# Kernel optimization log

Measured on AMD Instinct MI355X. Metric: run time of the kernel, lower is better.

Reference implementation:

```python
import jax, jax.numpy as jnp
import numpy as np

SMOOTHING = 0.9  # NEURON_CONFIG['signal_smoothing']
NUM_SOURCE = 16384
NUM_TARGET = 16384
NUM_BRANCHES = 64
BATCH = 32


def setup_inputs() -> dict:
    key = jax.random.key(0)
    k1, k2, k3, k4 = jax.random.split(key, 4)
    spikes = jax.random.normal(k1, (BATCH, NUM_SOURCE), dtype=jnp.float32)
    attenuation = jax.random.uniform(k2, (NUM_SOURCE, NUM_BRANCHES), dtype=jnp.float32)
    target_indices = jax.random.randint(k3, (NUM_SOURCE, NUM_BRANCHES), 0, NUM_TARGET)
    delays = jax.random.randint(k4, (NUM_SOURCE, NUM_BRANCHES), 0, 6)
    return {"spikes": spikes, "attenuation": attenuation,
            "target_indices": target_indices, "delays": delays}


def reference(spikes, attenuation, target_indices, delays):
    # spikes: [B, S]; attenuation/delays/target_indices: [S, Br]
    B = spikes.shape[0]
    num_target = NUM_TARGET
    att = jnp.clip(attenuation, 0.0, 1.0)
    decay = SMOOTHING ** delays.astype(spikes.dtype)          # [S, Br]
    # fused elementwise: signal per (batch, source, branch)
    signals = spikes[:, :, None] * (att * decay)[None, :, :]   # [B, S, Br]
    flat_t = target_indices.reshape(-1)                        # [S*Br]
    flat_s = signals.reshape(B, -1)                            # [B, S*Br]
    out = jnp.zeros((B, num_target), dtype=spikes.dtype)
    out = out.at[jnp.arange(B)[:, None], flat_t[None, :]].add(flat_s)
    return out
```

## Files before the change

### kernel.cpp

```cpp
#include <hip/hip_runtime.h>

#define S_  16384
#define T_  16384
#define B_  32
#define NEDGES (S_ * 64)
#define G_    256
#define NBKT  256
#define TPB   64
#define CAP_CELL  64
#define CAP_SPILL 64
#define CAP_BKT   6144

__device__ __forceinline__ float edge_weight(float a, int d) {
  float w = fminf(fmaxf(a, 0.0f), 1.0f);
  float r = (d & 1) ? 0.9f : 1.0f;
  r = (d & 2) ? r * 0.81f   : r;
  r = (d & 4) ? r * 0.6561f : r;
  return w * r;
}

__global__ __launch_bounds__(1024) void produce(
    const float* __restrict__ spikes,
    const float* __restrict__ att,
    const int*   __restrict__ tgt,
    const int*   __restrict__ del,
    float* __restrict__ spikesT,
    int2*  __restrict__ rec,
    int*   __restrict__ cntT,
    int*   __restrict__ spillCnt,
    int2*  __restrict__ spill) {
  __shared__ float tile[64][33];
  __shared__ int   cur[NBKT];
  __shared__ int   scur;
  const int g   = blockIdx.x;
  const int tid = threadIdx.x;

  if (tid < NBKT) cur[tid] = 0;
  if (tid == 0)   scur = 0;

  {
    const int x  = tid & 63;
    const int y  = tid >> 6;
    const int s0 = g * 64;
    tile[x][y]      = spikes[(size_t)y        * S_ + s0 + x];
    tile[x][y + 16] = spikes[(size_t)(y + 16) * S_ + s0 + x];
    __syncthreads();
    const int j = tid >> 5;
    const int b = tid & 31;
    spikesT[(size_t)(s0 + j)      * 32 + b] = tile[j][b];
    spikesT[(size_t)(s0 + j + 32) * 32 + b] = tile[j + 32][b];
  }

  const int e4  = g * 1024 + tid;
  int4   t = reinterpret_cast<const int4*>(tgt)[e4];
  float4 a = reinterpret_cast<const float4*>(att)[e4];
  int4   d = reinterpret_cast<const int4*>(del)[e4];
  const int src = (e4 * 4) >> 6;

#define EMIT(TV, AV, DV)                                                      \
  {                                                                           \
    const int bkt = (TV) >> 6;                                                \
    const int tl  = (TV) & 63;                                                \
    const int wb  = __float_as_int(edge_weight((AV), (DV)));                  \
    int slot = __hip_atomic_fetch_add(&cur[bkt], 1, __ATOMIC_RELAXED,         \
                                      __HIP_MEMORY_SCOPE_WORKGROUP);          \
    if (slot < CAP_CELL) {                                                    \
      rec[(((size_t)((bkt << 8) | g)) << 6) + slot] =                         \
          make_int2((tl << 14) | src, wb);                                    \
    } else {                                                                  \
      int sp = __hip_atomic_fetch_add(&scur, 1, __ATOMIC_RELAXED,             \
                                      __HIP_MEMORY_SCOPE_WORKGROUP);          \
      if (sp < CAP_SPILL)                                                     \
        spill[g * CAP_SPILL + sp] =                                           \
            make_int2((bkt << 20) | (tl << 14) | src, wb);                    \
    }                                                                         \
  }
  EMIT(t.x, a.x, d.x)
  EMIT(t.y, a.y, d.y)
  EMIT(t.z, a.z, d.z)
  EMIT(t.w, a.w, d.w)
#undef EMIT

  __syncthreads();
  if (tid < NBKT) cntT[tid * G_ + g] = min(cur[tid], CAP_CELL);
  if (tid == 0)   spillCnt[g] = min(scur, CAP_SPILL);
}

__global__ __launch_bounds__(1024) void consume(
    const int2* __restrict__ rec,
    const int*  __restrict__ cntT,
    const int*  __restrict__ spillCnt,
    const int2* __restrict__ spill,
    const float* __restrict__ spikesT,
    float* __restrict__ out) {
  __shared__ int2  srt[CAP_BKT];
  __shared__ float otile[64][33];
  __shared__ int   ccnt[NBKT], cexc[NBKT], sa[NBKT];
  __shared__ int   h64[TPB], ofs65[TPB + 1], cur64[TPB];
  __shared__ int   ntot_sh, spill_tot;

  const int k   = blockIdx.x;
  const int tid = threadIdx.x;
  const int b   = tid & 31;
  const int hw  = tid >> 5;

  if (tid < NBKT) ccnt[tid] = cntT[k * G_ + tid];
  if (tid < TPB)  h64[tid] = 0;
  if (tid == 0)   spill_tot = 0;
  __syncthreads();

  if (tid < NBKT) sa[tid] = ccnt[tid];
  __syncthreads();
  for (int o = 1; o < NBKT; o <<= 1) {
    int v = 0;
    if (tid < NBKT) { v = sa[tid]; if (tid >= o) v += sa[tid - o]; }
    __syncthreads();
    if (tid < NBKT) sa[tid] = v;
    __syncthreads();
  }
  if (tid < NBKT) cexc[tid] = (tid == 0) ? 0 : sa[tid - 1];
  if (tid == 0)   ntot_sh = sa[NBKT - 1];
  __syncthreads();
  const int ntot = min(ntot_sh, CAP_BKT);

  for (int g = hw; g < NBKT; g += 32) {
    const int n = ccnt[g];
    const int2* cell = rec + (((size_t)((k << 8) | g)) << 6);
    for (int j = b; j < n; j += 32)
      __hip_atomic_fetch_add(&h64[(cell[j].x >> 14) & 63], 1, __ATOMIC_RELAXED,
                             __HIP_MEMORY_SCOPE_WORKGROUP);
  }
  __syncthreads();

  if (tid < TPB) sa[tid] = h64[tid];
  __syncthreads();
  for (int o = 1; o < TPB; o <<= 1) {
    int v = 0;
    if (tid < TPB) { v = sa[tid]; if (tid >= o) v += sa[tid - o]; }
    __syncthreads();
    if (tid < TPB) sa[tid] = v;
    __syncthreads();
  }
  if (tid < TPB) {
    int e = (tid == 0) ? 0 : sa[tid - 1];
    ofs65[tid] = e;
    cur64[tid] = e;
  }
  if (tid == 0) ofs65[TPB] = sa[TPB - 1];
  __syncthreads();

  for (int g = hw; g < NBKT; g += 32) {
    const int n = ccnt[g];
    const int2* cell = rec + (((size_t)((k << 8) | g)) << 6);
    for (int j = b; j < n; j += 32) {
      int2 r = cell[j];
      const int tl = (r.x >> 14) & 63;
      int p = __hip_atomic_fetch_add(&cur64[tl], 1, __ATOMIC_RELAXED,
                                     __HIP_MEMORY_SCOPE_WORKGROUP);
      if (p < CAP_BKT) srt[p] = make_int2(r.x & 0x3FFF, r.y);
    }
  }
  __syncthreads();

  float acc0 = 0.f, acc1 = 0.f;
#pragma unroll
  for (int u = 0; u < 2; ++u) {
    const int t  = hw + u * 32;
    int e        = ofs65[t];
    const int e1 = min(ofs65[t + 1], ntot);
    float acc = 0.f;
    for (; e + 2 <= e1; e += 2) {
      int2 r0 = srt[e];
      int2 r1 = srt[e + 1];
      acc = fmaf(__int_as_float(r0.y), spikesT[(size_t)r0.x * 32 + b], acc);
      acc = fmaf(__int_as_float(r1.y), spikesT[(size_t)r1.x * 32 + b], acc);
    }
    if (e < e1) {
      int2 r = srt[e];
      acc = fmaf(__int_as_float(r.y), spikesT[(size_t)r.x * 32 + b], acc);
    }
    if (u == 0) acc0 = acc; else acc1 = acc;
  }

  if (tid < NBKT) sa[tid] = spillCnt[tid];
  __syncthreads();
  if (tid < NBKT && sa[tid] > 0)
    __hip_atomic_fetch_add(&spill_tot, sa[tid], __ATOMIC_RELAXED,
                           __HIP_MEMORY_SCOPE_WORKGROUP);
  __syncthreads();
  if (spill_tot > 0) {
    for (int g = 0; g < NBKT; ++g) {
      const int n = sa[g];
      for (int j = 0; j < n; ++j) {
        int2 r = spill[g * CAP_SPILL + j];
        if ((r.x >> 20) == k) {
          const int tl = (r.x >> 14) & 63;
          const float v = __int_as_float(r.y) *
                          spikesT[(size_t)(r.x & 0x3FFF) * 32 + b];
          if (tl == hw)      acc0 += v;
          else if (tl == hw + 32) acc1 += v;
        }
      }
    }
  }

  __syncthreads();
  otile[hw][b]      = acc0;
  otile[hw + 32][b] = acc1;
  __syncthreads();
  const int r = tid >> 5;
  const int c = (tid & 31) * 2;
  float2 o2 = make_float2(otile[c][r], otile[c + 1][r]);
  *reinterpret_cast<float2*>(&out[(size_t)r * T_ + k * 64 + c]) = o2;
}

__global__ void zero_floats(float* __restrict__ p, int n) {
  int i = blockIdx.x * blockDim.x + threadIdx.x;
  if (i < n) p[i] = 0.0f;
}

__global__ void naive_kernel(const float* __restrict__ spikes,
                             const float* __restrict__ att,
                             const int*   __restrict__ tgt,
                             const int*   __restrict__ del,
                             float*       __restrict__ out) {
  int i = blockIdx.x * blockDim.x + threadIdx.x;
  if (i >= NEDGES) return;
  int   s = i >> 6;
  int   t = tgt[i];
  float w = edge_weight(att[i], del[i]);
  for (int b = 0; b < B_; ++b)
    unsafeAtomicAdd(&out[(size_t)b * T_ + t], w * spikes[(size_t)b * S_ + s]);
}

extern "C" void kernel_launch(void* const* d_in, const int* in_sizes, int n_in,
                              void* d_out, int out_size, void* d_ws, size_t ws_size,
                              hipStream_t stream) {
  const float* spikes = (const float*)d_in[0];
  const float* att    = (const float*)d_in[1];
  const int*   tgt    = (const int*)d_in[2];
  const int*   del    = (const int*)d_in[3];
  float*       out    = (float*)d_out;

  const size_t spikesT_bytes = (size_t)S_ * B_ * sizeof(float);
  const size_t rec_bytes     = (size_t)NBKT * G_ * CAP_CELL * sizeof(int2);
  const size_t cnt_bytes     = (size_t)NBKT * G_ * sizeof(int);
  const size_t spillc_bytes  = (size_t)G_ * sizeof(int);
  const size_t spill_bytes   = (size_t)G_ * CAP_SPILL * sizeof(int2);
  const size_t need = spikesT_bytes + rec_bytes + cnt_bytes + spillc_bytes +
                      spill_bytes + 64;

  if (ws_size < need) {
    zero_floats<<<(B_ * T_ + 255) / 256, 256, 0, stream>>>(out, B_ * T_);
    naive_kernel<<<(NEDGES + 255) / 256, 256, 0, stream>>>(spikes, att, tgt, del, out);
    return;
  }

  char* p = (char*)d_ws;
  float* spikesT  = (float*)p;  p += spikesT_bytes;
  int2*  rec      = (int2*)p;   p += rec_bytes;
  int*   cntT     = (int*)p;    p += cnt_bytes;
  int*   spillCnt = (int*)p;    p += spillc_bytes;
  int2*  spill    = (int2*)p;

  produce<<<G_, 1024, 0, stream>>>(spikes, att, tgt, del,
                                   spikesT, rec, cntT, spillCnt, spill);
  consume<<<NBKT, 1024, 0, stream>>>(rec, cntT, spillCnt, spill, spikesT, out);
}
```

Before: 106.1 us.

## Shrink bucket cells and embed counts in record slot zero for one-cell-per-thread consume

Doubles the producer and consumer grids to 512 blocks of 512 threads, with buckets of 32 targets and cells capped at 16 entries. The per-cell count now lives in slot 0 of each record cell, so the separate count array and the consumer's 256-wide prefix scan go away. Each consumer thread loads its whole cell with vector int4 reads and keeps it in registers for both the histogram and scatter passes, and a wave shuffle scan replaces the shared-memory scan. The risk is that the small cells overflow more often, which pushes more records into the serial spill path that every consume block walks across all 512 producers.

```diff
diff --git a/kernel.cpp b/kernel.cpp
--- a/kernel.cpp
+++ b/kernel.cpp
@@ -1,15 +1,15 @@
 #include <hip/hip_runtime.h>
 
-#define S_  16384
-#define T_  16384
-#define B_  32
+#define S_   16384
+#define T_   16384
+#define B_   32
 #define NEDGES (S_ * 64)
-#define G_    256
-#define NBKT  256
-#define TPB   64
-#define CAP_CELL  64
-#define CAP_SPILL 64
-#define CAP_BKT   6144
+#define GP_  512
+#define NBKT 512
+#define TPB  32
+#define CAP_CELL  16
+#define CAP_SPILL 16
+#define CAP_SRT   2560
 
 __device__ __forceinline__ float edge_weight(float a, int d) {
   float w = fminf(fmaxf(a, 0.0f), 1.0f);
@@ -19,39 +19,38 @@
   return w * r;
 }
 
-__global__ __launch_bounds__(1024) void produce(
+__global__ __launch_bounds__(512) void produce(
     const float* __restrict__ spikes,
     const float* __restrict__ att,
     const int*   __restrict__ tgt,
     const int*   __restrict__ del,
     float* __restrict__ spikesT,
     int2*  __restrict__ rec,
-    int*   __restrict__ cntT,
     int*   __restrict__ spillCnt,
     int2*  __restrict__ spill) {
-  __shared__ float tile[64][33];
+  __shared__ float tile[32][33];
   __shared__ int   cur[NBKT];
   __shared__ int   scur;
   const int g   = blockIdx.x;
   const int tid = threadIdx.x;
 
-  if (tid < NBKT) cur[tid] = 0;
-  if (tid == 0)   scur = 0;
-
+  cur[tid] = 1;
+  if (tid == 0) scur = 0;
+
+  const int s0 = g * 32;
   {
-    const int x  = tid & 63;
-    const int y  = tid >> 6;
-    const int s0 = g * 64;
+    const int x = tid & 31;
+    const int y = tid >> 5;
     tile[x][y]      = spikes[(size_t)y        * S_ + s0 + x];
     tile[x][y + 16] = spikes[(size_t)(y + 16) * S_ + s0 + x];
     __syncthreads();
+    const int b = tid & 31;
     const int j = tid >> 5;
-    const int b = tid & 31;
     spikesT[(size_t)(s0 + j)      * 32 + b] = tile[j][b];
-    spikesT[(size_t)(s0 + j + 32) * 32 + b] = tile[j + 32][b];
-  }
-
-  const int e4  = g * 1024 + tid;
+    spikesT[(size_t)(s0 + j + 16) * 32 + b] = tile[j + 16][b];
+  }
+
+  const int e4  = g * 512 + tid;
   int4   t = reinterpret_cast<const int4*>(tgt)[e4];
   float4 a = reinterpret_cast<const float4*>(att)[e4];
   int4   d = reinterpret_cast<const int4*>(del)[e4];
@@ -59,20 +58,20 @@
 
 #define EMIT(TV, AV, DV)                                                      \
   {                                                                           \
-    const int bkt = (TV) >> 6;                                                \
-    const int tl  = (TV) & 63;                                                \
+    const int bkt = (TV) >> 5;                                                \
+    const int tl  = (TV) & 31;                                                \
     const int wb  = __float_as_int(edge_weight((AV), (DV)));                  \
     int slot = __hip_atomic_fetch_add(&cur[bkt], 1, __ATOMIC_RELAXED,         \
                                       __HIP_MEMORY_SCOPE_WORKGROUP);          \
     if (slot < CAP_CELL) {                                                    \
-      rec[(((size_t)((bkt << 8) | g)) << 6) + slot] =                         \
+      rec[(((size_t)((bkt << 9) | g)) << 4) + slot] =                         \
           make_int2((tl << 14) | src, wb);                                    \
     } else {                                                                  \
       int sp = __hip_atomic_fetch_add(&scur, 1, __ATOMIC_RELAXED,             \
                                       __HIP_MEMORY_SCOPE_WORKGROUP);          \
       if (sp < CAP_SPILL)                                                     \
         spill[g * CAP_SPILL + sp] =                                           \
-            make_int2((bkt << 20) | (tl << 14) | src, wb);                    \
+            make_int2((bkt << 19) | (tl << 14) | src, wb);                    \
     }                                                                         \
   }
   EMIT(t.x, a.x, d.x)
@@ -82,136 +81,149 @@
 #undef EMIT
 
   __syncthreads();
-  if (tid < NBKT) cntT[tid * G_ + g] = min(cur[tid], CAP_CELL);
-  if (tid == 0)   spillCnt[g] = min(scur, CAP_SPILL);
-}
-
-__global__ __launch_bounds__(1024) void consume(
+  rec[((size_t)((tid << 9) | g)) << 4] = make_int2(min(cur[tid] - 1, 15), 0);
+  if (tid == 0) spillCnt[g] = min(scur, CAP_SPILL);
+}
+
+__global__ __launch_bounds__(512) void consume(
     const int2* __restrict__ rec,
-    const int*  __restrict__ cntT,
     const int*  __restrict__ spillCnt,
     const int2* __restrict__ spill,
     const float* __restrict__ spikesT,
     float* __restrict__ out) {
-  __shared__ int2  srt[CAP_BKT];
-  __shared__ float otile[64][33];
-  __shared__ int   ccnt[NBKT], cexc[NBKT], sa[NBKT];
-  __shared__ int   h64[TPB], ofs65[TPB + 1], cur64[TPB];
-  __shared__ int   ntot_sh, spill_tot;
+  __shared__ int2  srt[CAP_SRT];
+  __shared__ float otile[TPB][33];
+  __shared__ int   h32[TPB], ofs[TPB + 1], cur32[TPB];
+  __shared__ int   spill_any;
 
   const int k   = blockIdx.x;
   const int tid = threadIdx.x;
   const int b   = tid & 31;
   const int hw  = tid >> 5;
 
-  if (tid < NBKT) ccnt[tid] = cntT[k * G_ + tid];
-  if (tid < TPB)  h64[tid] = 0;
-  if (tid == 0)   spill_tot = 0;
-  __syncthreads();
-
-  if (tid < NBKT) sa[tid] = ccnt[tid];
-  __syncthreads();
-  for (int o = 1; o < NBKT; o <<= 1) {
-    int v = 0;
-    if (tid < NBKT) { v = sa[tid]; if (tid >= o) v += sa[tid - o]; }
-    __syncthreads();
-    if (tid < NBKT) sa[tid] = v;
-    __syncthreads();
-  }
-  if (tid < NBKT) cexc[tid] = (tid == 0) ? 0 : sa[tid - 1];
-  if (tid == 0)   ntot_sh = sa[NBKT - 1];
-  __syncthreads();
-  const int ntot = min(ntot_sh, CAP_BKT);
-
-  for (int g = hw; g < NBKT; g += 32) {
-    const int n = ccnt[g];
-    const int2* cell = rec + (((size_t)((k << 8) | g)) << 6);
-    for (int j = b; j < n; j += 32)
-      __hip_atomic_fetch_add(&h64[(cell[j].x >> 14) & 63], 1, __ATOMIC_RELAXED,
+  if (tid < TPB) h32[tid] = 0;
+  if (tid == 0)  spill_any = 0;
+  const int myspill = spillCnt[tid];
+  __syncthreads();
+  if (myspill)
+    __hip_atomic_fetch_add(&spill_any, myspill, __ATOMIC_RELAXED,
+                           __HIP_MEMORY_SCOPE_WORKGROUP);
+
+  const int4* cp = reinterpret_cast<const int4*>(
+      rec + (((size_t)((k << 9) | tid)) << 4));
+  int4 c0 = cp[0], c1 = cp[1], c2 = cp[2], c3 = cp[3];
+  const int n = min(c0.x, 15);
+  int2 lo[7] = {{c0.z, c0.w}, {c1.x, c1.y}, {c1.z, c1.w},
+                {c2.x, c2.y}, {c2.z, c2.w}, {c3.x, c3.y}, {c3.z, c3.w}};
+  int2 hi[8];
+  if (n > 7) {
+    int4 c4 = cp[4], c5 = cp[5], c6 = cp[6], c7 = cp[7];
+    hi[0] = {c4.x, c4.y}; hi[1] = {c4.z, c4.w};
+    hi[2] = {c5.x, c5.y}; hi[3] = {c5.z, c5.w};
+    hi[4] = {c6.x, c6.y}; hi[5] = {c6.z, c6.w};
+    hi[6] = {c7.x, c7.y}; hi[7] = {c7.z, c7.w};
+  }
+
+#pragma unroll
+  for (int j = 0; j < 7; ++j)
+    if (j < n)
+      __hip_atomic_fetch_add(&h32[(lo[j].x >> 14) & 31], 1, __ATOMIC_RELAXED,
                              __HIP_MEMORY_SCOPE_WORKGROUP);
-  }
-  __syncthreads();
-
-  if (tid < TPB) sa[tid] = h64[tid];
-  __syncthreads();
-  for (int o = 1; o < TPB; o <<= 1) {
-    int v = 0;
-    if (tid < TPB) { v = sa[tid]; if (tid >= o) v += sa[tid - o]; }
-    __syncthreads();
-    if (tid < TPB) sa[tid] = v;
-    __syncthreads();
-  }
-  if (tid < TPB) {
-    int e = (tid == 0) ? 0 : sa[tid - 1];
-    ofs65[tid] = e;
-    cur64[tid] = e;
-  }
-  if (tid == 0) ofs65[TPB] = sa[TPB - 1];
-  __syncthreads();
-
-  for (int g = hw; g < NBKT; g += 32) {
-    const int n = ccnt[g];
-    const int2* cell = rec + (((size_t)((k << 8) | g)) << 6);
-    for (int j = b; j < n; j += 32) {
-      int2 r = cell[j];
-      const int tl = (r.x >> 14) & 63;
-      int p = __hip_atomic_fetch_add(&cur64[tl], 1, __ATOMIC_RELAXED,
+  if (n > 7) {
+#pragma unroll
+    for (int j = 0; j < 8; ++j)
+      if (7 + j < n)
+        __hip_atomic_fetch_add(&h32[(hi[j].x >> 14) & 31], 1, __ATOMIC_RELAXED,
+                               __HIP_MEMORY_SCOPE_WORKGROUP);
+  }
+  __syncthreads();
+
+  if (tid < 32) {
+    int v = h32[tid];
+    const int orig = v;
+#pragma unroll
+    for (int off = 1; off < 32; off <<= 1) {
+      int u = __shfl_up(v, off);
+      if (tid >= off) v += u;
+    }
+    ofs[tid]   = v - orig;
+    cur32[tid] = v - orig;
+    if (tid == 31) ofs[32] = v;
+  }
+  __syncthreads();
+
+#pragma unroll
+  for (int j = 0; j < 7; ++j)
+    if (j < n) {
+      int2 r = lo[j];
+      int p = __hip_atomic_fetch_add(&cur32[(r.x >> 14) & 31], 1,
+                                     __ATOMIC_RELAXED,
                                      __HIP_MEMORY_SCOPE_WORKGROUP);
-      if (p < CAP_BKT) srt[p] = make_int2(r.x & 0x3FFF, r.y);
-    }
+      if (p < CAP_SRT) srt[p] = make_int2(r.x & 0x3FFF, r.y);
+    }
+  if (n > 7) {
+#pragma unroll
+    for (int j = 0; j < 8; ++j)
+      if (7 + j < n) {
+        int2 r = hi[j];
+        int p = __hip_atomic_fetch_add(&cur32[(r.x >> 14) & 31], 1,
+                                       __ATOMIC_RELAXED,
+                                       __HIP_MEMORY_SCOPE_WORKGROUP);
+        if (p < CAP_SRT) srt[p] = make_int2(r.x & 0x3FFF, r.y);
+      }
   }
   __syncthreads();
 
   float acc0 = 0.f, acc1 = 0.f;
-#pragma unroll
-  for (int u = 0; u < 2; ++u) {
-    const int t  = hw + u * 32;
-    int e        = ofs65[t];
-    const int e1 = min(ofs65[t + 1], ntot);
-    float acc = 0.f;
+  {
+    int e        = ofs[hw];
+    const int e1 = ofs[hw + 1];
     for (; e + 2 <= e1; e += 2) {
-      int2 r0 = srt[e];
-      int2 r1 = srt[e + 1];
-      acc = fmaf(__int_as_float(r0.y), spikesT[(size_t)r0.x * 32 + b], acc);
-      acc = fmaf(__int_as_float(r1.y), spikesT[(size_t)r1.x * 32 + b], acc);
+      int2 r0 = srt[e], r1 = srt[e + 1];
+      acc0 = fmaf(__int_as_float(r0.y), spikesT[(size_t)r0.x * 32 + b], acc0);
+      acc0 = fmaf(__int_as_float(r1.y), spikesT[(size_t)r1.x * 32 + b], acc0);
     }
     if (e < e1) {
       int2 r = srt[e];
-      acc = fmaf(__int_as_float(r.y), spikesT[(size_t)r.x * 32 + b], acc);
-    }
-    if (u == 0) acc0 = acc; else acc1 = acc;
-  }
-
-  if (tid < NBKT) sa[tid] = spillCnt[tid];
-  __syncthreads();
-  if (tid < NBKT && sa[tid] > 0)
-    __hip_atomic_fetch_add(&spill_tot, sa[tid], __ATOMIC_RELAXED,
-                           __HIP_MEMORY_SCOPE_WORKGROUP);
-  __syncthreads();
-  if (spill_tot > 0) {
-    for (int g = 0; g < NBKT; ++g) {
-      const int n = sa[g];
-      for (int j = 0; j < n; ++j) {
-        int2 r = spill[g * CAP_SPILL + j];
-        if ((r.x >> 20) == k) {
-          const int tl = (r.x >> 14) & 63;
-          const float v = __int_as_float(r.y) *
-                          spikesT[(size_t)(r.x & 0x3FFF) * 32 + b];
-          if (tl == hw)      acc0 += v;
-          else if (tl == hw + 32) acc1 += v;
-        }
+      acc0 = fmaf(__int_as_float(r.y), spikesT[(size_t)r.x * 32 + b], acc0);
+    }
+  }
+  {
+    int e        = ofs[hw + 16];
+    const int e1 = ofs[hw + 17];
+    for (; e + 2 <= e1; e += 2) {
+      int2 r0 = srt[e], r1 = srt[e + 1];
+      acc1 = fmaf(__int_as_float(r0.y), spikesT[(size_t)r0.x * 32 + b], acc1);
+      acc1 = fmaf(__int_as_float(r1.y), spikesT[(size_t)r1.x * 32 + b], acc1);
+    }
+    if (e < e1) {
+      int2 r = srt[e];
+      acc1 = fmaf(__int_as_float(r.y), spikesT[(size_t)r.x * 32 + b], acc1);
+    }
+  }
+
+  if (spill_any > 0) {
+    for (int g2 = 0; g2 < GP_; ++g2) {
+      const int ns = spillCnt[g2];
+      for (int j = 0; j < ns; ++j) {
+        int2 e = spill[g2 * CAP_SPILL + j];
+        if ((e.x >> 19) != k) continue;
+        const int tl = (e.x >> 14) & 31;
+        const float v = __int_as_float(e.y) *
+                        spikesT[(size_t)(e.x & 0x3FFF) * 32 + b];
+        if (tl == hw)           acc0 += v;
+        else if (tl == hw + 16) acc1 += v;
       }
     }
   }
 
-  __syncthreads();
   otile[hw][b]      = acc0;
-  otile[hw + 32][b] = acc1;
-  __syncthreads();
-  const int r = tid >> 5;
-  const int c = (tid & 31) * 2;
-  float2 o2 = make_float2(otile[c][r], otile[c + 1][r]);
-  *reinterpret_cast<float2*>(&out[(size_t)r * T_ + k * 64 + c]) = o2;
+  otile[hw + 16][b] = acc1;
+  __syncthreads();
+  const int bb = tid >> 4;
+  const int cc = (tid & 15) * 2;
+  float2 o2 = make_float2(otile[cc][bb], otile[cc + 1][bb]);
+  *reinterpret_cast<float2*>(&out[(size_t)bb * T_ + k * 32 + cc]) = o2;
 }
 
 __global__ void zero_floats(float* __restrict__ p, int n) {
@@ -243,12 +255,10 @@
   float*       out    = (float*)d_out;
 
   const size_t spikesT_bytes = (size_t)S_ * B_ * sizeof(float);
-  const size_t rec_bytes     = (size_t)NBKT * G_ * CAP_CELL * sizeof(int2);
-  const size_t cnt_bytes     = (size_t)NBKT * G_ * sizeof(int);
-  const size_t spillc_bytes  = (size_t)G_ * sizeof(int);
-  const size_t spill_bytes   = (size_t)G_ * CAP_SPILL * sizeof(int2);
-  const size_t need = spikesT_bytes + rec_bytes + cnt_bytes + spillc_bytes +
-                      spill_bytes + 64;
+  const size_t rec_bytes     = (size_t)NBKT * GP_ * CAP_CELL * sizeof(int2);
+  const size_t spillc_bytes  = (size_t)GP_ * sizeof(int);
+  const size_t spill_bytes   = (size_t)GP_ * CAP_SPILL * sizeof(int2);
+  const size_t need = spikesT_bytes + rec_bytes + spillc_bytes + spill_bytes + 64;
 
   if (ws_size < need) {
     zero_floats<<<(B_ * T_ + 255) / 256, 256, 0, stream>>>(out, B_ * T_);
@@ -259,11 +269,10 @@
   char* p = (char*)d_ws;
   float* spikesT  = (float*)p;  p += spikesT_bytes;
   int2*  rec      = (int2*)p;   p += rec_bytes;
-  int*   cntT     = (int*)p;    p += cnt_bytes;
   int*   spillCnt = (int*)p;    p += spillc_bytes;
   int2*  spill    = (int2*)p;
 
-  produce<<<G_, 1024, 0, stream>>>(spikes, att, tgt, del,
-                                   spikesT, rec, cntT, spillCnt, spill);
-  consume<<<NBKT, 1024, 0, stream>>>(rec, cntT, spillCnt, spill, spikesT, out);
-}
+  produce<<<GP_, 512, 0, stream>>>(spikes, att, tgt, del,
+                                   spikesT, rec, spillCnt, spill);
+  consume<<<NBKT, 512, 0, stream>>>(rec, spillCnt, spill, spikesT, out);
+}
```

Result: slower. 141.1 us (+32.9%).
